# Optimization experiments

Measured on AMD Instinct MI355X. Metric: run time of the kernel, lower is better.

Reference implementation:

```python
import jax, jax.numpy as jnp
import numpy as np

VOCAB_SIZE = 53
HIDDEN = 2048
LAYERS = 6


def setup_inputs() -> dict:
    key = jax.random.key(0)
    ks = jax.random.split(key, 9)
    s = 0.02
    inp = {
        "input": jax.random.randint(ks[0], (1,), 0, VOCAB_SIZE),
        "hidden": jax.random.normal(ks[1], (LAYERS, 1, HIDDEN), dtype=jnp.float32),
        "emb": jax.random.normal(ks[2], (VOCAB_SIZE, HIDDEN), dtype=jnp.float32) * s,
        "w_ih": jax.random.normal(ks[3], (LAYERS, 3 * HIDDEN, HIDDEN), dtype=jnp.float32) * s,
        "w_hh": jax.random.normal(ks[4], (LAYERS, 3 * HIDDEN, HIDDEN), dtype=jnp.float32) * s,
        "b_ih": jax.random.normal(ks[5], (LAYERS, 3 * HIDDEN), dtype=jnp.float32) * s,
        "b_hh": jax.random.normal(ks[6], (LAYERS, 3 * HIDDEN), dtype=jnp.float32) * s,
        "w_dec": jax.random.normal(ks[7], (VOCAB_SIZE, HIDDEN), dtype=jnp.float32) * s,
        "b_dec": jax.random.normal(ks[8], (VOCAB_SIZE,), dtype=jnp.float32) * s,
    }
    return inp


def _gru_stack(x, h, w_ih, w_hh, b_ih, b_hh):
    # x: [H] layer-0 input; h: [L,H]; weights stacked over layers.
    # PyTorch GRU cell: r,z,n gates, n uses r * (W_hn h + b_hn).
    def step(x_l, params):
        h_l, wi, wh, bi, bh = params
        gi = wi @ x_l + bi            # [3H]
        gh = wh @ h_l + bh            # [3H]
        i_r, i_z, i_n = jnp.split(gi, 3)
        h_r, h_z, h_n = jnp.split(gh, 3)
        r = jax.nn.sigmoid(i_r + h_r)
        z = jax.nn.sigmoid(i_z + h_z)
        n = jnp.tanh(i_n + r * h_n)
        h_new = (1.0 - z) * n + z * h_l
        return h_new, h_new
    x_out, h_new = jax.lax.scan(step, x, (h, w_ih, w_hh, b_ih, b_hh))
    return x_out, h_new


def reference(input, hidden, emb, w_ih, w_hh, b_ih, b_hh, w_dec, b_dec):
    x = emb[input[0]]                 # [H] embedding lookup
    h = hidden[:, 0, :]               # [L,H]
    x_out, h_new = _gru_stack(x, h, w_ih, w_hh, b_ih, b_hh)
    logits = (w_dec @ x_out + b_dec)[None, :]   # [1, vocab]
    return logits, h_new[:, None, :]            # ([1,V], [L,1,H])
```

## Files before the change

### kernel.cpp

```cpp
#include <hip/hip_runtime.h>
#include <hip/hip_bf16.h>

#define HIDDEN   2048
#define GROWS    6144
#define VOCAB    53
#define LAYERS   6
#define NBLK     512
#define NT       768
#define JPB      4

typedef unsigned long long ull;

#define WS_H_OFF     0
#define WS_SUB_OFF   49152
#define SUB_LINES    32
#define BLK_PER_SUB  (NBLK / SUB_LINES)
#define WS_MST_OFF   (WS_SUB_OFF + SUB_LINES * 64 * LAYERS)
#define WS_CTR_BYTES (SUB_LINES * 64 * LAYERS + 64 * LAYERS)

__global__ __launch_bounds__(NT, 6) void gru_fused(
    const int*   __restrict__ token,
    const float* __restrict__ hidden,
    const float* __restrict__ emb,
    const float* __restrict__ w_ih,
    const float* __restrict__ w_hh,
    const float* __restrict__ b_ih,
    const float* __restrict__ b_hh,
    const float* __restrict__ w_dec,
    const float* __restrict__ b_dec,
    float*       __restrict__ out,
    char*        __restrict__ ws)
{
    const int bid  = blockIdx.x;
    const int tid  = threadIdx.x;
    const int wave = tid >> 6;
    const int lane = tid & 63;
    const int g    = wave >> 2;
    const int k    = wave & 3;
    const int j    = bid + NBLK * k;

    float*    h_work = (float*)(ws + WS_H_OFF);
    unsigned* subc   = (unsigned*)(ws + WS_SUB_OFF);
    unsigned* mstc   = (unsigned*)(ws + WS_MST_OFF);

    __shared__ float xlds[HIDDEN];
    __shared__ float rgh[2][3][JPB];
    __shared__ float rgi[2][3][JPB];

    const size_t rowoff = ((size_t)g * HIDDEN + (size_t)j) * HIDDEN;
    const float* x0 = emb + (size_t)token[0] * HIDDEN;

    for (int l = 0; l < LAYERS; ++l) {
        const int p = l & 1;

        {
            const float4* W = (const float4*)(w_hh + (size_t)l * GROWS * HIDDEN + rowoff);
            const float4* v = (const float4*)(hidden + (size_t)l * HIDDEN);
            float s = 0.f;
            #pragma unroll
            for (int it = 0; it < 8; ++it) {
                float4 a = W[lane + 64 * it];
                float4 b = v[lane + 64 * it];
                s += a.x * b.x + a.y * b.y + a.z * b.z + a.w * b.w;
            }
            #pragma unroll
            for (int o = 32; o; o >>= 1) s += __shfl_down(s, o, 64);
            if (lane == 0) rgh[p][g][k] = s;
        }

        float4 wf[8];
        {
            const float4* W = (const float4*)(w_ih + (size_t)l * GROWS * HIDDEN + rowoff);
            #pragma unroll
            for (int it = 0; it < 8; ++it) wf[it] = W[lane + 64 * it];
        }

        if (l > 0 && tid == 0) {
            while (__hip_atomic_load(&mstc[(l - 1) * 16], __ATOMIC_RELAXED,
                                     __HIP_MEMORY_SCOPE_AGENT) < (unsigned)SUB_LINES)
                __builtin_amdgcn_s_sleep(8);
        }
        __syncthreads();

        if (l == 0) {
            const ull* src = (const ull*)x0;
            for (int i = tid; i < HIDDEN / 2; i += NT)
                ((ull*)xlds)[i] = src[i];
        } else {
            const ull* src = (const ull*)(h_work + (size_t)(l - 1) * HIDDEN);
            for (int i = tid; i < HIDDEN / 2; i += NT)
                ((ull*)xlds)[i] = __hip_atomic_load(&src[i], __ATOMIC_RELAXED,
                                                    __HIP_MEMORY_SCOPE_AGENT);
        }
        __syncthreads();

        {
            const float4* xl = (const float4*)xlds;
            float s = 0.f;
            #pragma unroll
            for (int it = 0; it < 8; ++it) {
                float4 b = xl[lane + 64 * it];
                s += wf[it].x * b.x + wf[it].y * b.y + wf[it].z * b.z + wf[it].w * b.w;
            }
            #pragma unroll
            for (int o = 32; o; o >>= 1) s += __shfl_down(s, o, 64);
            if (lane == 0) rgi[p][g][k] = s;
        }
        __syncthreads();

        if (wave == 0) {
            if (lane < JPB) {
                const int jj = bid + NBLK * lane;
                const float* bi = b_ih + (size_t)l * GROWS;
                const float* bh = b_hh + (size_t)l * GROWS;
                float gir = rgi[p][0][lane] + bi[jj];
                float giz = rgi[p][1][lane] + bi[jj + HIDDEN];
                float gin = rgi[p][2][lane] + bi[jj + 2 * HIDDEN];
                float ghr = rgh[p][0][lane] + bh[jj];
                float ghz = rgh[p][1][lane] + bh[jj + HIDDEN];
                float ghn = rgh[p][2][lane] + bh[jj + 2 * HIDDEN];
                float r = 1.f / (1.f + __expf(-(gir + ghr)));
                float z = 1.f / (1.f + __expf(-(giz + ghz)));
                float n = tanhf(gin + r * ghn);
                float hv = (1.f - z) * n + z * hidden[(size_t)l * HIDDEN + jj];
                __hip_atomic_store(&h_work[(size_t)l * HIDDEN + jj], hv,
                                   __ATOMIC_RELAXED, __HIP_MEMORY_SCOPE_AGENT);
                out[VOCAB + (size_t)l * HIDDEN + jj] = hv;
            }
            asm volatile("s_waitcnt vmcnt(0)" ::: "memory");
            if (lane == 0) {
                unsigned old = __hip_atomic_fetch_add(
                    &subc[(l * SUB_LINES + (bid & (SUB_LINES - 1))) * 16], 1u,
                    __ATOMIC_RELAXED, __HIP_MEMORY_SCOPE_AGENT);
                if (old == (unsigned)(BLK_PER_SUB - 1))
                    __hip_atomic_fetch_add(&mstc[l * 16], 1u,
                                           __ATOMIC_RELAXED, __HIP_MEMORY_SCOPE_AGENT);
            }
        }
    }

    if (bid < VOCAB) {
        if (tid == 0) {
            while (__hip_atomic_load(&mstc[(LAYERS - 1) * 16], __ATOMIC_RELAXED,
                                     __HIP_MEMORY_SCOPE_AGENT) < (unsigned)SUB_LINES)
                __builtin_amdgcn_s_sleep(8);
        }
        __syncthreads();
        {
            const ull* src = (const ull*)(h_work + (size_t)(LAYERS - 1) * HIDDEN);
            for (int i = tid; i < HIDDEN / 2; i += NT)
                ((ull*)xlds)[i] = __hip_atomic_load(&src[i], __ATOMIC_RELAXED,
                                                    __HIP_MEMORY_SCOPE_AGENT);
        }
        __syncthreads();
        const float4* W  = (const float4*)(w_dec + (size_t)bid * HIDDEN);
        const float4* xl = (const float4*)xlds;
        float s = 0.f;
        if (tid < 512) {
            float4 a = W[tid];
            float4 b = xl[tid];
            s = a.x * b.x + a.y * b.y + a.z * b.z + a.w * b.w;
        }
        #pragma unroll
        for (int o = 32; o; o >>= 1) s += __shfl_down(s, o, 64);
        __shared__ float dred[12];
        if (lane == 0) dred[wave] = s;
        __syncthreads();
        if (tid == 0) {
            float t = 0.f;
            #pragma unroll
            for (int w = 0; w < 12; ++w) t += dred[w];
            out[bid] = t + b_dec[bid];
        }
    }
}

extern "C" void kernel_launch(void* const* d_in, const int* in_sizes, int n_in,
                              void* d_out, int out_size, void* d_ws, size_t ws_size,
                              hipStream_t stream) {
    const int*   token  = (const int*)  d_in[0];
    const float* hidden = (const float*)d_in[1];
    const float* emb    = (const float*)d_in[2];
    const float* w_ih   = (const float*)d_in[3];
    const float* w_hh   = (const float*)d_in[4];
    const float* b_ih   = (const float*)d_in[5];
    const float* b_hh   = (const float*)d_in[6];
    const float* w_dec  = (const float*)d_in[7];
    const float* b_dec  = (const float*)d_in[8];

    float* out = (float*)d_out;
    char*  ws  = (char*)d_ws;

    (void)hipMemsetAsync(ws + WS_SUB_OFF, 0, WS_CTR_BYTES, stream);

    gru_fused<<<dim3(NBLK), dim3(NT), 0, stream>>>(
        token, hidden, emb, w_ih, w_hh, b_ih, b_hh,
        w_dec, b_dec, out, ws);
}
```

Before: 130.9 us.

## Assign one hidden unit per wave with all three gates per wave

Restructures the per-layer GRU work so each wave computes all three gate rows of one hidden unit, for both w_hh and w_ih. Blocks shrink from 768 to 256 threads, which removes the cross-wave LDS gate exchange and two block barriers. The two-level counter scheme (sub-counters plus a master counter) is replaced by wave 0 polling all 32 sub-counters in parallel with a short sleep, and a per-block LDS counter signals layer completion. Each wave now holds 24 float4 of w_ih in registers, which raises register pressure, and occupancy drops to a launch bound of 2 blocks.

```diff
diff --git a/kernel.cpp b/kernel.cpp
--- a/kernel.cpp
+++ b/kernel.cpp
@@ -1,24 +1,24 @@
 #include <hip/hip_runtime.h>
-#include <hip/hip_bf16.h>
 
 #define HIDDEN   2048
 #define GROWS    6144
 #define VOCAB    53
 #define LAYERS   6
 #define NBLK     512
-#define NT       768
-#define JPB      4
-
-typedef unsigned long long ull;
+#define NWAVE    4
+#define NT       256
+#define SUB_LINES   32
+#define BLK_PER_SUB (NBLK / SUB_LINES)
 
 #define WS_H_OFF     0
 #define WS_SUB_OFF   49152
-#define SUB_LINES    32
-#define BLK_PER_SUB  (NBLK / SUB_LINES)
-#define WS_MST_OFF   (WS_SUB_OFF + SUB_LINES * 64 * LAYERS)
-#define WS_CTR_BYTES (SUB_LINES * 64 * LAYERS + 64 * LAYERS)
-
-__global__ __launch_bounds__(NT, 6) void gru_fused(
+#define WS_CTR_BYTES (SUB_LINES * 64 * LAYERS)
+
+typedef unsigned long long ull;
+
+#define VMCNT0 asm volatile("s_waitcnt vmcnt(0)" ::: "memory")
+
+__global__ __launch_bounds__(NT, 2) void gru_fused(
     const int*   __restrict__ token,
     const float* __restrict__ hidden,
     const float* __restrict__ emb,
@@ -35,143 +35,170 @@
     const int tid  = threadIdx.x;
     const int wave = tid >> 6;
     const int lane = tid & 63;
-    const int g    = wave >> 2;
-    const int k    = wave & 3;
-    const int j    = bid + NBLK * k;
+    const int j    = bid * NWAVE + wave;
 
     float*    h_work = (float*)(ws + WS_H_OFF);
     unsigned* subc   = (unsigned*)(ws + WS_SUB_OFF);
-    unsigned* mstc   = (unsigned*)(ws + WS_MST_OFF);
-
-    __shared__ float xlds[HIDDEN];
-    __shared__ float rgh[2][3][JPB];
-    __shared__ float rgi[2][3][JPB];
-
-    const size_t rowoff = ((size_t)g * HIDDEN + (size_t)j) * HIDDEN;
+
+    __shared__ float    xlds[HIDDEN];
+    __shared__ unsigned done[LAYERS];
+    if (tid < LAYERS) done[tid] = 0;
+    __syncthreads();
+
     const float* x0 = emb + (size_t)token[0] * HIDDEN;
 
     for (int l = 0; l < LAYERS; ++l) {
-        const int p = l & 1;
-
+        const float* Whh = w_hh + (size_t)l * GROWS * HIDDEN;
+        const float* Wih = w_ih + (size_t)l * GROWS * HIDDEN;
+
+        float4 hv[8];
         {
-            const float4* W = (const float4*)(w_hh + (size_t)l * GROWS * HIDDEN + rowoff);
-            const float4* v = (const float4*)(hidden + (size_t)l * HIDDEN);
+            const float4* hs = (const float4*)(hidden + (size_t)l * HIDDEN);
+            #pragma unroll
+            for (int u = 0; u < 8; ++u) hv[u] = hs[u * 64 + lane];
+        }
+
+        float ah[3];
+        #pragma unroll
+        for (int gt = 0; gt < 3; ++gt) {
+            const float4* W = (const float4*)(Whh + ((size_t)gt * HIDDEN + j) * HIDDEN);
             float s = 0.f;
             #pragma unroll
-            for (int it = 0; it < 8; ++it) {
-                float4 a = W[lane + 64 * it];
-                float4 b = v[lane + 64 * it];
-                s += a.x * b.x + a.y * b.y + a.z * b.z + a.w * b.w;
-            }
-            #pragma unroll
-            for (int o = 32; o; o >>= 1) s += __shfl_down(s, o, 64);
-            if (lane == 0) rgh[p][g][k] = s;
-        }
-
-        float4 wf[8];
-        {
-            const float4* W = (const float4*)(w_ih + (size_t)l * GROWS * HIDDEN + rowoff);
-            #pragma unroll
-            for (int it = 0; it < 8; ++it) wf[it] = W[lane + 64 * it];
-        }
-
-        if (l > 0 && tid == 0) {
-            while (__hip_atomic_load(&mstc[(l - 1) * 16], __ATOMIC_RELAXED,
-                                     __HIP_MEMORY_SCOPE_AGENT) < (unsigned)SUB_LINES)
-                __builtin_amdgcn_s_sleep(8);
+            for (int u = 0; u < 8; ++u) {
+                float4 w4 = W[u * 64 + lane];
+                s += w4.x * hv[u].x + w4.y * hv[u].y + w4.z * hv[u].z + w4.w * hv[u].w;
+            }
+            ah[gt] = s;
+        }
+
+        float4 wf[3][8];
+        #pragma unroll
+        for (int gt = 0; gt < 3; ++gt) {
+            const float4* W = (const float4*)(Wih + ((size_t)gt * HIDDEN + j) * HIDDEN);
+            #pragma unroll
+            for (int u = 0; u < 8; ++u) wf[gt][u] = W[u * 64 + lane];
+        }
+
+        if (l > 0 && wave == 0) {
+            const unsigned* sc = subc + (size_t)(l - 1) * SUB_LINES * 16;
+            for (;;) {
+                unsigned c = BLK_PER_SUB;
+                if (lane < SUB_LINES)
+                    c = __hip_atomic_load(&sc[lane * 16], __ATOMIC_RELAXED,
+                                          __HIP_MEMORY_SCOPE_AGENT);
+                if (__all(c >= BLK_PER_SUB)) break;
+                __builtin_amdgcn_s_sleep(1);
+            }
         }
         __syncthreads();
 
         if (l == 0) {
-            const ull* src = (const ull*)x0;
-            for (int i = tid; i < HIDDEN / 2; i += NT)
-                ((ull*)xlds)[i] = src[i];
+            const float4* xs = (const float4*)x0;
+            #pragma unroll
+            for (int i = 0; i < 2; ++i)
+                ((float4*)xlds)[tid + i * NT] = xs[tid + i * NT];
         } else {
-            const ull* src = (const ull*)(h_work + (size_t)(l - 1) * HIDDEN);
-            for (int i = tid; i < HIDDEN / 2; i += NT)
-                ((ull*)xlds)[i] = __hip_atomic_load(&src[i], __ATOMIC_RELAXED,
-                                                    __HIP_MEMORY_SCOPE_AGENT);
-        }
-        __syncthreads();
-
+            const ull* hsrc = (const ull*)(h_work + (size_t)(l - 1) * HIDDEN);
+            #pragma unroll
+            for (int i = 0; i < 4; ++i)
+                ((ull*)xlds)[tid + i * NT] =
+                    __hip_atomic_load(&hsrc[tid + i * NT], __ATOMIC_RELAXED,
+                                      __HIP_MEMORY_SCOPE_AGENT);
+        }
+        __syncthreads();
+
+        float ai[3];
         {
             const float4* xl = (const float4*)xlds;
-            float s = 0.f;
-            #pragma unroll
-            for (int it = 0; it < 8; ++it) {
-                float4 b = xl[lane + 64 * it];
-                s += wf[it].x * b.x + wf[it].y * b.y + wf[it].z * b.z + wf[it].w * b.w;
-            }
-            #pragma unroll
-            for (int o = 32; o; o >>= 1) s += __shfl_down(s, o, 64);
-            if (lane == 0) rgi[p][g][k] = s;
-        }
-        __syncthreads();
-
+            float4 xv[8];
+            #pragma unroll
+            for (int u = 0; u < 8; ++u) xv[u] = xl[u * 64 + lane];
+            #pragma unroll
+            for (int gt = 0; gt < 3; ++gt) {
+                float s = 0.f;
+                #pragma unroll
+                for (int u = 0; u < 8; ++u)
+                    s += wf[gt][u].x * xv[u].x + wf[gt][u].y * xv[u].y
+                       + wf[gt][u].z * xv[u].z + wf[gt][u].w * xv[u].w;
+                ai[gt] = s;
+            }
+        }
+
+        #pragma unroll
+        for (int o = 32; o; o >>= 1) {
+            ah[0] += __shfl_down(ah[0], o, 64);
+            ah[1] += __shfl_down(ah[1], o, 64);
+            ah[2] += __shfl_down(ah[2], o, 64);
+            ai[0] += __shfl_down(ai[0], o, 64);
+            ai[1] += __shfl_down(ai[1], o, 64);
+            ai[2] += __shfl_down(ai[2], o, 64);
+        }
+
+        if (lane == 0) {
+            const float* bi = b_ih + (size_t)l * GROWS;
+            const float* bh = b_hh + (size_t)l * GROWS;
+            float gir = ai[0] + bi[j];
+            float giz = ai[1] + bi[j + HIDDEN];
+            float gin = ai[2] + bi[j + 2 * HIDDEN];
+            float ghr = ah[0] + bh[j];
+            float ghz = ah[1] + bh[j + HIDDEN];
+            float ghn = ah[2] + bh[j + 2 * HIDDEN];
+            float r = 1.f / (1.f + __expf(-(gir + ghr)));
+            float z = 1.f / (1.f + __expf(-(giz + ghz)));
+            float n = tanhf(gin + r * ghn);
+            float hvv = (1.f - z) * n + z * hidden[(size_t)l * HIDDEN + j];
+            __hip_atomic_store(&h_work[(size_t)l * HIDDEN + j], hvv,
+                               __ATOMIC_RELAXED, __HIP_MEMORY_SCOPE_AGENT);
+            out[VOCAB + (size_t)l * HIDDEN + j] = hvv;
+        }
+        VMCNT0;
+        if (lane == 0) {
+            unsigned old = atomicAdd(&done[l], 1u);
+            if (old == NWAVE - 1)
+                __hip_atomic_fetch_add(
+                    &subc[((size_t)l * SUB_LINES + (bid & (SUB_LINES - 1))) * 16],
+                    1u, __ATOMIC_RELAXED, __HIP_MEMORY_SCOPE_AGENT);
+        }
+    }
+
+    if (bid < VOCAB) {
         if (wave == 0) {
-            if (lane < JPB) {
-                const int jj = bid + NBLK * lane;
-                const float* bi = b_ih + (size_t)l * GROWS;
-                const float* bh = b_hh + (size_t)l * GROWS;
-                float gir = rgi[p][0][lane] + bi[jj];
-                float giz = rgi[p][1][lane] + bi[jj + HIDDEN];
-                float gin = rgi[p][2][lane] + bi[jj + 2 * HIDDEN];
-                float ghr = rgh[p][0][lane] + bh[jj];
-                float ghz = rgh[p][1][lane] + bh[jj + HIDDEN];
-                float ghn = rgh[p][2][lane] + bh[jj + 2 * HIDDEN];
-                float r = 1.f / (1.f + __expf(-(gir + ghr)));
-                float z = 1.f / (1.f + __expf(-(giz + ghz)));
-                float n = tanhf(gin + r * ghn);
-                float hv = (1.f - z) * n + z * hidden[(size_t)l * HIDDEN + jj];
-                __hip_atomic_store(&h_work[(size_t)l * HIDDEN + jj], hv,
-                                   __ATOMIC_RELAXED, __HIP_MEMORY_SCOPE_AGENT);
-                out[VOCAB + (size_t)l * HIDDEN + jj] = hv;
-            }
-            asm volatile("s_waitcnt vmcnt(0)" ::: "memory");
-            if (lane == 0) {
-                unsigned old = __hip_atomic_fetch_add(
-                    &subc[(l * SUB_LINES + (bid & (SUB_LINES - 1))) * 16], 1u,
-                    __ATOMIC_RELAXED, __HIP_MEMORY_SCOPE_AGENT);
-                if (old == (unsigned)(BLK_PER_SUB - 1))
-                    __hip_atomic_fetch_add(&mstc[l * 16], 1u,
-                                           __ATOMIC_RELAXED, __HIP_MEMORY_SCOPE_AGENT);
-            }
-        }
-    }
-
-    if (bid < VOCAB) {
-        if (tid == 0) {
-            while (__hip_atomic_load(&mstc[(LAYERS - 1) * 16], __ATOMIC_RELAXED,
-                                     __HIP_MEMORY_SCOPE_AGENT) < (unsigned)SUB_LINES)
-                __builtin_amdgcn_s_sleep(8);
+            const unsigned* sc = subc + (size_t)(LAYERS - 1) * SUB_LINES * 16;
+            for (;;) {
+                unsigned c = BLK_PER_SUB;
+                if (lane < SUB_LINES)
+                    c = __hip_atomic_load(&sc[lane * 16], __ATOMIC_RELAXED,
+                                          __HIP_MEMORY_SCOPE_AGENT);
+                if (__all(c >= BLK_PER_SUB)) break;
+                __builtin_amdgcn_s_sleep(1);
+            }
         }
         __syncthreads();
         {
-            const ull* src = (const ull*)(h_work + (size_t)(LAYERS - 1) * HIDDEN);
-            for (int i = tid; i < HIDDEN / 2; i += NT)
-                ((ull*)xlds)[i] = __hip_atomic_load(&src[i], __ATOMIC_RELAXED,
-                                                    __HIP_MEMORY_SCOPE_AGENT);
+            const ull* hsrc = (const ull*)(h_work + (size_t)(LAYERS - 1) * HIDDEN);
+            #pragma unroll
+            for (int i = 0; i < 4; ++i)
+                ((ull*)xlds)[tid + i * NT] =
+                    __hip_atomic_load(&hsrc[tid + i * NT], __ATOMIC_RELAXED,
+                                      __HIP_MEMORY_SCOPE_AGENT);
         }
         __syncthreads();
         const float4* W  = (const float4*)(w_dec + (size_t)bid * HIDDEN);
         const float4* xl = (const float4*)xlds;
         float s = 0.f;
-        if (tid < 512) {
-            float4 a = W[tid];
-            float4 b = xl[tid];
-            s = a.x * b.x + a.y * b.y + a.z * b.z + a.w * b.w;
+        #pragma unroll
+        for (int i = 0; i < 2; ++i) {
+            float4 a = W[tid + i * NT];
+            float4 b = xl[tid + i * NT];
+            s += a.x * b.x + a.y * b.y + a.z * b.z + a.w * b.w;
         }
         #pragma unroll
         for (int o = 32; o; o >>= 1) s += __shfl_down(s, o, 64);
-        __shared__ float dred[12];
+        __shared__ float dred[NWAVE];
         if (lane == 0) dred[wave] = s;
         __syncthreads();
-        if (tid == 0) {
-            float t = 0.f;
-            #pragma unroll
-            for (int w = 0; w < 12; ++w) t += dred[w];
-            out[bid] = t + b_dec[bid];
-        }
+        if (tid == 0)
+            out[bid] = dred[0] + dred[1] + dred[2] + dred[3] + b_dec[bid];
     }
 }
 
```

Measured after the change: 161.0 us. +23.0%, slower.

## Replace two-level barrier counter with wave-wide polling of sub-counters and prefetch biases

Applied to the files above, without the earlier changes.

Drops the master counter so the last arriver no longer does a second atomic; instead a whole wave polls all 32 sub-counters in parallel and exits when every one is full, with a shorter sleep. Bias and previous-hidden loads are hoisted ahead of the barrier, and the w_hh reduction is moved after the w_ih prefetch so the loads overlap. The decoder reads the final hidden state straight from global instead of staging it in LDS. The cost is more polling traffic on the counter lines from 512 blocks.

```diff
diff --git a/kernel.cpp b/kernel.cpp
--- a/kernel.cpp
+++ b/kernel.cpp
@@ -1,22 +1,27 @@
 #include <hip/hip_runtime.h>
-#include <hip/hip_bf16.h>
 
 #define HIDDEN   2048
 #define GROWS    6144
 #define VOCAB    53
 #define LAYERS   6
 #define NBLK     512
+#define NWAVE    12
 #define NT       768
 #define JPB      4
-
-typedef unsigned long long ull;
+#define SUB_LINES   32
+#define BLK_PER_SUB (NBLK / SUB_LINES)
 
 #define WS_H_OFF     0
 #define WS_SUB_OFF   49152
-#define SUB_LINES    32
-#define BLK_PER_SUB  (NBLK / SUB_LINES)
-#define WS_MST_OFF   (WS_SUB_OFF + SUB_LINES * 64 * LAYERS)
-#define WS_CTR_BYTES (SUB_LINES * 64 * LAYERS + 64 * LAYERS)
+#define WS_CTR_BYTES (SUB_LINES * 64 * LAYERS)
+
+typedef unsigned long long ull;
+#define PIN_VM asm volatile("s_waitcnt vmcnt(0)" ::: "memory")
+union FU { ull u; float2 f; };
+
+__device__ __forceinline__ float dot4(float4 a, float4 b) {
+    return a.x * b.x + a.y * b.y + a.z * b.z + a.w * b.w;
+}
 
 __global__ __launch_bounds__(NT, 6) void gru_fused(
     const int*   __restrict__ token,
@@ -36,140 +41,147 @@
     const int wave = tid >> 6;
     const int lane = tid & 63;
     const int g    = wave >> 2;
-    const int k    = wave & 3;
-    const int j    = bid + NBLK * k;
+    const int slot = wave & 3;
+    const int j    = bid + NBLK * slot;
 
     float*    h_work = (float*)(ws + WS_H_OFF);
     unsigned* subc   = (unsigned*)(ws + WS_SUB_OFF);
-    unsigned* mstc   = (unsigned*)(ws + WS_MST_OFF);
 
     __shared__ float xlds[HIDDEN];
-    __shared__ float rgh[2][3][JPB];
-    __shared__ float rgi[2][3][JPB];
-
-    const size_t rowoff = ((size_t)g * HIDDEN + (size_t)j) * HIDDEN;
+    __shared__ float rgh[3][JPB];
+    __shared__ float rgi[3][JPB];
+
     const float* x0 = emb + (size_t)token[0] * HIDDEN;
 
     for (int l = 0; l < LAYERS; ++l) {
-        const int p = l & 1;
-
+        const size_t lbase = (size_t)l * GROWS * HIDDEN;
+        const size_t roff  = ((size_t)g * HIDDEN + (size_t)j) * HIDDEN;
+
+        float a = 0.f;
         {
-            const float4* W = (const float4*)(w_hh + (size_t)l * GROWS * HIDDEN + rowoff);
-            const float4* v = (const float4*)(hidden + (size_t)l * HIDDEN);
-            float s = 0.f;
-            #pragma unroll
-            for (int it = 0; it < 8; ++it) {
-                float4 a = W[lane + 64 * it];
-                float4 b = v[lane + 64 * it];
-                s += a.x * b.x + a.y * b.y + a.z * b.z + a.w * b.w;
-            }
-            #pragma unroll
-            for (int o = 32; o; o >>= 1) s += __shfl_down(s, o, 64);
-            if (lane == 0) rgh[p][g][k] = s;
+            const float4* W  = (const float4*)(w_hh + lbase + roff);
+            const float4* Hs = (const float4*)(hidden + (size_t)l * HIDDEN);
+            #pragma unroll
+            for (int u = 0; u < 8; ++u)
+                a += dot4(W[u * 64 + lane], Hs[u * 64 + lane]);
+        }
+
+        float bir = 0.f, biz = 0.f, bin = 0.f, bhr = 0.f, bhz = 0.f, bhn = 0.f,
+              hprev = 0.f;
+        if (wave == 0 && lane < JPB) {
+            const int jj = bid + NBLK * lane;
+            const float* bi = b_ih + (size_t)l * GROWS;
+            const float* bh = b_hh + (size_t)l * GROWS;
+            bir = bi[jj]; biz = bi[jj + HIDDEN]; bin = bi[jj + 2 * HIDDEN];
+            bhr = bh[jj]; bhz = bh[jj + HIDDEN]; bhn = bh[jj + 2 * HIDDEN];
+            hprev = hidden[(size_t)l * HIDDEN + jj];
         }
 
         float4 wf[8];
         {
-            const float4* W = (const float4*)(w_ih + (size_t)l * GROWS * HIDDEN + rowoff);
-            #pragma unroll
-            for (int it = 0; it < 8; ++it) wf[it] = W[lane + 64 * it];
-        }
-
-        if (l > 0 && tid == 0) {
-            while (__hip_atomic_load(&mstc[(l - 1) * 16], __ATOMIC_RELAXED,
-                                     __HIP_MEMORY_SCOPE_AGENT) < (unsigned)SUB_LINES)
-                __builtin_amdgcn_s_sleep(8);
+            const float4* Wi = (const float4*)(w_ih + lbase + roff);
+            #pragma unroll
+            for (int u = 0; u < 8; ++u) wf[u] = Wi[u * 64 + lane];
+        }
+        PIN_VM;
+
+        #pragma unroll
+        for (int o = 32; o; o >>= 1) a += __shfl_down(a, o, 64);
+
+        if (l > 0 && wave == 0) {
+            const unsigned* sc = subc + (size_t)(l - 1) * SUB_LINES * 16;
+            for (;;) {
+                unsigned c = BLK_PER_SUB;
+                if (lane < SUB_LINES)
+                    c = __hip_atomic_load(&sc[lane * 16], __ATOMIC_RELAXED,
+                                          __HIP_MEMORY_SCOPE_AGENT);
+                if (__all(c >= BLK_PER_SUB)) break;
+                __builtin_amdgcn_s_sleep(2);
+            }
         }
         __syncthreads();
 
         if (l == 0) {
-            const ull* src = (const ull*)x0;
             for (int i = tid; i < HIDDEN / 2; i += NT)
-                ((ull*)xlds)[i] = src[i];
+                ((ull*)xlds)[i] = ((const ull*)x0)[i];
         } else {
-            const ull* src = (const ull*)(h_work + (size_t)(l - 1) * HIDDEN);
+            const ull* hsrc = (const ull*)(h_work + (size_t)(l - 1) * HIDDEN);
             for (int i = tid; i < HIDDEN / 2; i += NT)
-                ((ull*)xlds)[i] = __hip_atomic_load(&src[i], __ATOMIC_RELAXED,
+                ((ull*)xlds)[i] = __hip_atomic_load(&hsrc[i], __ATOMIC_RELAXED,
                                                     __HIP_MEMORY_SCOPE_AGENT);
         }
         __syncthreads();
 
+        float c = 0.f;
         {
             const float4* xl = (const float4*)xlds;
-            float s = 0.f;
-            #pragma unroll
-            for (int it = 0; it < 8; ++it) {
-                float4 b = xl[lane + 64 * it];
-                s += wf[it].x * b.x + wf[it].y * b.y + wf[it].z * b.z + wf[it].w * b.w;
-            }
-            #pragma unroll
-            for (int o = 32; o; o >>= 1) s += __shfl_down(s, o, 64);
-            if (lane == 0) rgi[p][g][k] = s;
-        }
+            #pragma unroll
+            for (int u = 0; u < 8; ++u) c += dot4(wf[u], xl[u * 64 + lane]);
+        }
+        #pragma unroll
+        for (int o = 32; o; o >>= 1) c += __shfl_down(c, o, 64);
+
+        if (lane == 0) { rgh[g][slot] = a; rgi[g][slot] = c; }
         __syncthreads();
 
         if (wave == 0) {
             if (lane < JPB) {
                 const int jj = bid + NBLK * lane;
-                const float* bi = b_ih + (size_t)l * GROWS;
-                const float* bh = b_hh + (size_t)l * GROWS;
-                float gir = rgi[p][0][lane] + bi[jj];
-                float giz = rgi[p][1][lane] + bi[jj + HIDDEN];
-                float gin = rgi[p][2][lane] + bi[jj + 2 * HIDDEN];
-                float ghr = rgh[p][0][lane] + bh[jj];
-                float ghz = rgh[p][1][lane] + bh[jj + HIDDEN];
-                float ghn = rgh[p][2][lane] + bh[jj + 2 * HIDDEN];
+                float gir = rgi[0][lane] + bir;
+                float giz = rgi[1][lane] + biz;
+                float gin = rgi[2][lane] + bin;
+                float ghr = rgh[0][lane] + bhr;
+                float ghz = rgh[1][lane] + bhz;
+                float ghn = rgh[2][lane] + bhn;
                 float r = 1.f / (1.f + __expf(-(gir + ghr)));
                 float z = 1.f / (1.f + __expf(-(giz + ghz)));
                 float n = tanhf(gin + r * ghn);
-                float hv = (1.f - z) * n + z * hidden[(size_t)l * HIDDEN + jj];
+                float hv = (1.f - z) * n + z * hprev;
                 __hip_atomic_store(&h_work[(size_t)l * HIDDEN + jj], hv,
                                    __ATOMIC_RELAXED, __HIP_MEMORY_SCOPE_AGENT);
                 out[VOCAB + (size_t)l * HIDDEN + jj] = hv;
             }
-            asm volatile("s_waitcnt vmcnt(0)" ::: "memory");
-            if (lane == 0) {
-                unsigned old = __hip_atomic_fetch_add(
-                    &subc[(l * SUB_LINES + (bid & (SUB_LINES - 1))) * 16], 1u,
-                    __ATOMIC_RELAXED, __HIP_MEMORY_SCOPE_AGENT);
-                if (old == (unsigned)(BLK_PER_SUB - 1))
-                    __hip_atomic_fetch_add(&mstc[l * 16], 1u,
-                                           __ATOMIC_RELAXED, __HIP_MEMORY_SCOPE_AGENT);
+            PIN_VM;
+            if (lane == 0)
+                __hip_atomic_fetch_add(
+                    &subc[((size_t)l * SUB_LINES + (bid & (SUB_LINES - 1))) * 16],
+                    1u, __ATOMIC_RELAXED, __HIP_MEMORY_SCOPE_AGENT);
+        }
+    }
+
+    if (bid < VOCAB) {
+        if (wave == 0) {
+            const unsigned* sc = subc + (size_t)(LAYERS - 1) * SUB_LINES * 16;
+            for (;;) {
+                unsigned c = BLK_PER_SUB;
+                if (lane < SUB_LINES)
+                    c = __hip_atomic_load(&sc[lane * 16], __ATOMIC_RELAXED,
+                                          __HIP_MEMORY_SCOPE_AGENT);
+                if (__all(c >= BLK_PER_SUB)) break;
+                __builtin_amdgcn_s_sleep(2);
             }
         }
-    }
-
-    if (bid < VOCAB) {
-        if (tid == 0) {
-            while (__hip_atomic_load(&mstc[(LAYERS - 1) * 16], __ATOMIC_RELAXED,
-                                     __HIP_MEMORY_SCOPE_AGENT) < (unsigned)SUB_LINES)
-                __builtin_amdgcn_s_sleep(8);
-        }
-        __syncthreads();
-        {
-            const ull* src = (const ull*)(h_work + (size_t)(LAYERS - 1) * HIDDEN);
-            for (int i = tid; i < HIDDEN / 2; i += NT)
-                ((ull*)xlds)[i] = __hip_atomic_load(&src[i], __ATOMIC_RELAXED,
-                                                    __HIP_MEMORY_SCOPE_AGENT);
-        }
-        __syncthreads();
-        const float4* W  = (const float4*)(w_dec + (size_t)bid * HIDDEN);
-        const float4* xl = (const float4*)xlds;
+        __syncthreads();
         float s = 0.f;
         if (tid < 512) {
-            float4 a = W[tid];
-            float4 b = xl[tid];
-            s = a.x * b.x + a.y * b.y + a.z * b.z + a.w * b.w;
+            float4 a = ((const float4*)(w_dec + (size_t)bid * HIDDEN))[tid];
+            const ull* hsrc = (const ull*)(h_work + (size_t)(LAYERS - 1) * HIDDEN);
+            FU A, B;
+            A.u = __hip_atomic_load(&hsrc[2 * tid], __ATOMIC_RELAXED,
+                                    __HIP_MEMORY_SCOPE_AGENT);
+            B.u = __hip_atomic_load(&hsrc[2 * tid + 1], __ATOMIC_RELAXED,
+                                    __HIP_MEMORY_SCOPE_AGENT);
+            s = a.x * A.f.x + a.y * A.f.y + a.z * B.f.x + a.w * B.f.y;
         }
         #pragma unroll
         for (int o = 32; o; o >>= 1) s += __shfl_down(s, o, 64);
-        __shared__ float dred[12];
+        __shared__ float dred[NWAVE];
         if (lane == 0) dred[wave] = s;
         __syncthreads();
         if (tid == 0) {
             float t = 0.f;
             #pragma unroll
-            for (int w = 0; w < 12; ++w) t += dred[w];
+            for (int w = 0; w < NWAVE; ++w) t += dred[w];
             out[bid] = t + b_dec[bid];
         }
     }
```

After: 171.7 us. +31.2%, slower.
